# Optimization experiments

Hardware: AMD Instinct MI355X
Metric: run time of the kernel (lower is better)

## Reference

```python
import jax, jax.numpy as jnp
import numpy as np

D_MODEL, D_K, D_V = 1024, 64, 64

def setup_inputs() -> dict:
    key = jax.random.key(0)
    ks = jax.random.split(key, 7)
    s = 1.0 / np.sqrt(D_MODEL)
    return {
        "x": jax.random.normal(ks[0], (4, 4096, D_MODEL), dtype=jnp.float32),
        "w_q": jax.random.normal(ks[1], (D_MODEL, D_K), dtype=jnp.float32) * s,
        "b_q": jnp.zeros((D_K,), dtype=jnp.float32),
        "w_k": jax.random.normal(ks[2], (D_MODEL, D_K), dtype=jnp.float32) * s,
        "b_k": jnp.zeros((D_K,), dtype=jnp.float32),
        "w_v": jax.random.normal(ks[3], (D_MODEL, D_V), dtype=jnp.float32) * s,
        "b_v": jnp.zeros((D_V,), dtype=jnp.float32),
    }

def reference(x, w_q, b_q, w_k, b_k, w_v, b_v):
    # x: [b, s, d_model]
    q = x @ w_q + b_q                      # [b, s, d_k]
    k = x @ w_k + b_k                      # [b, s, d_k]
    v = x @ w_v + b_v                      # [b, s, d_v]
    scores = jnp.einsum("bqd,bkd->bqk", q, k) / jnp.sqrt(jnp.float32(D_K))
    seq_len = scores.shape[-1]
    causal = jnp.tril(jnp.ones((seq_len, seq_len), dtype=bool))  # keep lower-tri
    scores = jnp.where(causal, scores, -jnp.inf)
    probs = jax.nn.softmax(scores, axis=-1)
    return jnp.einsum("bqk,bkd->bqd", probs, v)  # [b, s, d_v]
```

## Files before the change

kernel.cpp:

```cpp
#include <hip/hip_runtime.h>
#include <hip/hip_bf16.h>

using f32x4    = __attribute__((ext_vector_type(4))) float;
using f32x16   = __attribute__((ext_vector_type(16))) float;
using bf16x8   = __attribute__((ext_vector_type(8))) __bf16;
using ushort8  = __attribute__((ext_vector_type(8))) unsigned short;
using ushort4v = __attribute__((ext_vector_type(4))) unsigned short;
using uint4v   = __attribute__((ext_vector_type(4))) unsigned int;
using float4v  = __attribute__((ext_vector_type(4))) float;

#define LOG2E 1.44269504088896340736f
#define SHIFT_L2 5.77078016355585f

static __device__ __forceinline__ unsigned short f2bf(float f) {
  union { __hip_bfloat16 h; unsigned short u; } cv;
  cv.h = __float2bfloat16(f);
  return cv.u;
}
static __device__ __forceinline__ bf16x8 ld_bf8_g(const void* p) {
  ushort8 u = *(const ushort8*)p;
  return __builtin_bit_cast(bf16x8, u);
}
static __device__ __forceinline__ float fast_exp2(float x) {
#if __has_builtin(__builtin_amdgcn_exp2f)
  return __builtin_amdgcn_exp2f(x);
#else
  return exp2f(x);
#endif
}
static __device__ __forceinline__ unsigned int pk2(float a, float b) {
  return (unsigned int)f2bf(a) | ((unsigned int)f2bf(b) << 16);
}

__global__ __launch_bounds__(256) void wprep_kernel(
    const float* __restrict__ wq, const float* __restrict__ wk,
    const float* __restrict__ wv, unsigned short* __restrict__ Wfrag) {
  int idx = blockIdx.x * 256 + threadIdx.x;
  int col = idx >> 10;
  int k   = idx & 1023;
  const float* w = (col < 64) ? wq : (col < 128) ? wk : wv;
  int c = col & 63;
  int n = col >> 4, l15 = col & 15;
  int kk = k >> 5, lh = (k >> 3) & 3, e = k & 7;
  size_t elem = ((size_t)(n * 32 + kk) * 64 + lh * 16 + l15) * 8 + e;
  Wfrag[elem] = f2bf(w[k * 64 + c]);
}

__global__ __launch_bounds__(256, 2) void proj_kernel(
    const float* __restrict__ x, const unsigned short* __restrict__ Wfrag,
    const float* __restrict__ bq, const float* __restrict__ bk,
    const float* __restrict__ bv,
    unsigned short* __restrict__ qb, unsigned short* __restrict__ kreg,
    unsigned short* __restrict__ vreg) {
  __shared__ __align__(16) char As[2][32 * 128];
  int tid = threadIdx.x, wave = tid >> 6, lane = tid & 63;
  int rowBase = blockIdx.x * 32;
  int rhalf = (wave & 1) * 16;
  int nbase = (wave >> 1) * 6;
  int l15 = lane & 15, lh = lane >> 4;

  int arow = tid >> 3, ac0 = (tid & 7) * 8;
  const float* xp = x + (size_t)(rowBase + arow) * 1024 + ac0;
  int abyte = (arow * 128 + ac0 * 2) ^ ((arow & 7) << 4);
  const char* wfb = (const char*)Wfrag + (size_t)lane * 16;

  f32x4 acc[6];
#pragma unroll
  for (int i = 0; i < 6; ++i) acc[i] = (f32x4){0.f, 0.f, 0.f, 0.f};

  float4v aL[2], aH[2];
  bf16x8 B[2][12];

  aL[0] = *(const float4v*)(xp);
  aH[0] = *(const float4v*)(xp + 4);
#pragma unroll
  for (int j = 0; j < 6; ++j) {
    B[0][j * 2]     = ld_bf8_g(wfb + (((size_t)(nbase + j) * 32 + 0) << 10));
    B[0][j * 2 + 1] = ld_bf8_g(wfb + (((size_t)(nbase + j) * 32 + 1) << 10));
  }
  {
    ushort8 u;
#pragma unroll
    for (int e = 0; e < 4; ++e) { u[e] = f2bf(aL[0][e]); u[4 + e] = f2bf(aH[0][e]); }
    *(ushort8*)(As[0] + abyte) = u;
  }
  aL[1] = *(const float4v*)(xp + 64);
  aH[1] = *(const float4v*)(xp + 68);
  asm volatile("s_waitcnt lgkmcnt(0)" ::: "memory");
  __builtin_amdgcn_s_barrier();
  __builtin_amdgcn_sched_barrier(0);

#pragma unroll
  for (int kt = 0; kt < 16; ++kt) {
    const int cur = kt & 1, nxt = cur ^ 1;
    if (kt < 15) {
#pragma unroll
      for (int j = 0; j < 6; ++j) {
        B[nxt][j * 2]     = ld_bf8_g(wfb + (((size_t)(nbase + j) * 32 + 2 * (kt + 1)) << 10));
        B[nxt][j * 2 + 1] = ld_bf8_g(wfb + (((size_t)(nbase + j) * 32 + 2 * (kt + 1) + 1) << 10));
      }
    }
    {
      int row = rhalf + l15;
      bf16x8 a0 = ld_bf8_g(As[cur] + ((row * 128 + lh * 16) ^ ((row & 7) << 4)));
      bf16x8 a1 = ld_bf8_g(As[cur] + ((row * 128 + 64 + lh * 16) ^ ((row & 7) << 4)));
#pragma unroll
      for (int j = 0; j < 6; ++j) {
        acc[j] = __builtin_amdgcn_mfma_f32_16x16x32_bf16(a0, B[cur][j * 2], acc[j], 0, 0, 0);
        acc[j] = __builtin_amdgcn_mfma_f32_16x16x32_bf16(a1, B[cur][j * 2 + 1], acc[j], 0, 0, 0);
      }
    }
    if (kt < 15) {
      ushort8 u;
#pragma unroll
      for (int e = 0; e < 4; ++e) { u[e] = f2bf(aL[nxt][e]); u[4 + e] = f2bf(aH[nxt][e]); }
      *(ushort8*)(As[nxt] + abyte) = u;
      if (kt < 14) {
        aL[cur] = *(const float4v*)(xp + (kt + 2) * 64);
        aH[cur] = *(const float4v*)(xp + (kt + 2) * 64 + 4);
      }
      asm volatile("s_waitcnt lgkmcnt(0)" ::: "memory");
      __builtin_amdgcn_s_barrier();
      __builtin_amdgcn_sched_barrier(0);
    }
  }

#pragma unroll
  for (int cf = 0; cf < 6; ++cf) {
    int col = (nbase + cf) * 16 + l15;
    int sel = col >> 6, c64 = col & 63;
    const float* bias = (sel == 0) ? bq : (sel == 1) ? bk : bv;
    float bb = bias[c64];
    if (sel == 0) {
#pragma unroll
      for (int r = 0; r < 4; ++r) {
        int row = rowBase + rhalf + lh * 4 + r;
        qb[(size_t)row * 64 + c64] = f2bf((acc[cf][r] + bb) * (0.125f * LOG2E));
      }
    } else if (sel == 1) {
      int j16 = c64 >> 4, hik = (c64 >> 3) & 1, e = c64 & 7;
#pragma unroll
      for (int r = 0; r < 4; ++r) {
        int s = rowBase + rhalf + lh * 4 + r;
        int b = s >> 12, sl = s & 4095;
        int ch = sl >> 7, kvw = sl & 127;
        int kvq = kvw >> 5, lk = kvw & 31;
        size_t off = (((size_t)(b * 32 + ch)) << 14) + kvq * 4096 + j16 * 1024 +
                     (hik * 32 + lk) * 16 + e * 2;
        *(unsigned short*)((char*)kreg + off) = f2bf(acc[cf][r] + bb);
      }
    } else {
      ushort4v w;
#pragma unroll
      for (int r = 0; r < 4; ++r) w[r] = f2bf(acc[cf][r] + bb);
      int s0 = rowBase + rhalf + lh * 4;
      int b = s0 >> 12, sl = s0 & 4095;
      int ch = sl >> 7, kvw = sl & 127;
      int kvq = kvw >> 5, k5 = kvw & 31;
      int kj = k5 >> 4, hiv = (k5 >> 3) & 1, e0 = k5 & 7;
      int dt = c64 >> 5, lv = c64 & 31, f = kj * 2 + dt;
      size_t off = (((size_t)(b * 32 + ch)) << 14) + kvq * 4096 + f * 1024 +
                   (hiv * 32 + lv) * 16 + e0 * 2;
      *(ushort4v*)((char*)vreg + off) = w;
    }
  }
}

__global__ __launch_bounds__(64, 4) void attn_kernel(
    const unsigned short* __restrict__ qb, const unsigned short* __restrict__ kreg,
    const unsigned short* __restrict__ vreg, float* __restrict__ po,
    float* __restrict__ lo) {
  int lane = threadIdx.x & 63;
  int l31 = lane & 31, hi = lane >> 5;
  int wid = blockIdx.x;
  int T = 127 - (wid >> 5);
  int low = wid & 31;
  int batch = low & 3, ph = low >> 2;
  int Tq = T * 32;
  const size_t bO = (size_t)batch * 262144;
  const char* kb = (const char*)kreg + ((size_t)batch << 19);
  const char* vb = (const char*)vreg + ((size_t)batch << 19);

  const unsigned short* qp = qb + bO + (size_t)(Tq + l31) * 64 + hi * 8;
  bf16x8 qf0 = ld_bf8_g(qp);
  bf16x8 qf1 = ld_bf8_g(qp + 16);
  bf16x8 qf2 = ld_bf8_g(qp + 32);
  bf16x8 qf3 = ld_bf8_g(qp + 48);

  f32x16 o0, o1;
#pragma unroll
  for (int r = 0; r < 16; ++r) { o0[r] = 0.f; o1[r] = 0.f; }
  float lsum = 0.f;

#pragma unroll 1
  for (int st = ph; st <= T; st += 8) {
    size_t base = ((size_t)(st >> 2) << 14) + (st & 3) * 4096 + lane * 16;
    const char* kp = kb + base;
    const char* vp = vb + base;
    bf16x8 k0 = ld_bf8_g(kp);
    bf16x8 k1 = ld_bf8_g(kp + 1024);
    bf16x8 k2 = ld_bf8_g(kp + 2048);
    bf16x8 k3 = ld_bf8_g(kp + 3072);
    bf16x8 v0 = ld_bf8_g(vp);
    bf16x8 v1 = ld_bf8_g(vp + 1024);
    bf16x8 v2 = ld_bf8_g(vp + 2048);
    bf16x8 v3 = ld_bf8_g(vp + 3072);

    f32x16 sc;
#pragma unroll
    for (int r = 0; r < 16; ++r) sc[r] = 0.f;
    sc = __builtin_amdgcn_mfma_f32_32x32x16_bf16(k0, qf0, sc, 0, 0, 0);
    sc = __builtin_amdgcn_mfma_f32_32x32x16_bf16(k1, qf1, sc, 0, 0, 0);
    sc = __builtin_amdgcn_mfma_f32_32x32x16_bf16(k2, qf2, sc, 0, 0, 0);
    sc = __builtin_amdgcn_mfma_f32_32x32x16_bf16(k3, qf3, sc, 0, 0, 0);
    if (st == T) {
      int qg = Tq + l31;
#pragma unroll
      for (int r = 0; r < 16; ++r) {
        int kvg = 32 * st + (r & 3) + 8 * (r >> 2) + 4 * hi;
        if (kvg > qg) sc[r] = -3.0e38f;
      }
    }
    float pv[16];
#pragma unroll
    for (int r = 0; r < 16; ++r) {
      pv[r] = fast_exp2(sc[r] - SHIFT_L2);
      lsum += pv[r];
    }
#pragma unroll
    for (int kj = 0; kj < 2; ++kj) {
      const int R = 8 * kj;
      unsigned int A0 = pk2(pv[R + 0], pv[R + 1]);
      unsigned int A1 = pk2(pv[R + 2], pv[R + 3]);
      unsigned int B0 = pk2(pv[R + 4], pv[R + 5]);
      unsigned int B1 = pk2(pv[R + 6], pv[R + 7]);
      unsigned int s0 = hi ? A0 : B0;
      unsigned int s1 = hi ? A1 : B1;
      unsigned int r0 = __shfl_xor((int)s0, 32, 64);
      unsigned int r1 = __shfl_xor((int)s1, 32, 64);
      uint4v dw = {hi ? r0 : A0, hi ? r1 : A1, hi ? B0 : r0, hi ? B1 : r1};
      bf16x8 pa = __builtin_bit_cast(bf16x8, dw);
      if (kj == 0) {
        o0 = __builtin_amdgcn_mfma_f32_32x32x16_bf16(pa, v0, o0, 0, 0, 0);
        o1 = __builtin_amdgcn_mfma_f32_32x32x16_bf16(pa, v1, o1, 0, 0, 0);
      } else {
        o0 = __builtin_amdgcn_mfma_f32_32x32x16_bf16(pa, v2, o0, 0, 0, 0);
        o1 = __builtin_amdgcn_mfma_f32_32x32x16_bf16(pa, v3, o1, 0, 0, 0);
      }
    }
  }

  lsum += __shfl_xor(lsum, 32, 64);

  float* pdst = po + (size_t)ph * 1048576 + bO + (size_t)Tq * 64;
#pragma unroll
  for (int r = 0; r < 16; ++r) {
    int qloc = (r & 3) + 8 * (r >> 2) + 4 * hi;
    pdst[qloc * 64 + l31] = o0[r];
    pdst[qloc * 64 + 32 + l31] = o1[r];
  }
  if (hi == 0) lo[ph * 16384 + batch * 4096 + Tq + l31] = lsum;
}

__global__ __launch_bounds__(256) void merge_kernel(
    const float* __restrict__ po, const float* __restrict__ lo,
    float* __restrict__ out) {
  int i = blockIdx.x * 256 + threadIdx.x;
  int row = i >> 4;
  float4v a = ((const float4v*)po)[i];
  float L = lo[row];
#pragma unroll
  for (int ph = 1; ph < 8; ++ph) {
    a += ((const float4v*)po)[i + ph * 262144];
    L += lo[row + ph * 16384];
  }
  a *= (1.0f / L);
  ((float4v*)out)[i] = a;
}

extern "C" void kernel_launch(void* const* d_in, const int* in_sizes, int n_in,
                              void* d_out, int out_size, void* d_ws, size_t ws_size,
                              hipStream_t stream) {
  const float* x  = (const float*)d_in[0];
  const float* wq = (const float*)d_in[1];
  const float* bq = (const float*)d_in[2];
  const float* wk = (const float*)d_in[3];
  const float* bk = (const float*)d_in[4];
  const float* wv = (const float*)d_in[5];
  const float* bv = (const float*)d_in[6];

  unsigned short* Wfrag = (unsigned short*)d_ws;
  unsigned short* qbuf  = Wfrag + 192 * 1024;
  unsigned short* kreg  = qbuf + 16384 * 64;
  unsigned short* vreg  = kreg + 16384 * 64;
  float*          po    = (float*)(vreg + 16384 * 64);
  float*          lo    = po + 8 * 1048576;

  wprep_kernel<<<768, 256, 0, stream>>>(wq, wk, wv, Wfrag);
  proj_kernel<<<512, 256, 0, stream>>>(x, Wfrag, bq, bk, bv, qbuf, kreg, vreg);
  attn_kernel<<<4096, 64, 0, stream>>>(qbuf, kreg, vreg, po, lo);
  merge_kernel<<<1024, 256, 0, stream>>>(po, lo, (float*)d_out);
}
```

Before: 55.45 us.

## Restructure projection GEMM into single-wave blocks with register-direct A loads

The projection kernel goes from 256-thread blocks that stage 32 rows of x in double-buffered LDS behind barriers to single-wave blocks of 16 rows. Each wave now computes all 192 output columns. Each lane loads its own fp32 x fragments from global memory with 4-deep register prefetch and converts them to bf16 in registers, and B fragments use 2-deep prefetch. This removes LDS traffic and block barriers, but doubles the weight-fragment reads from L2 per output row and leaves fewer waves per CU to hide memory latency.

```diff
diff --git a/kernel.cpp b/kernel.cpp
--- a/kernel.cpp
+++ b/kernel.cpp
@@ -46,102 +46,73 @@
   Wfrag[elem] = f2bf(w[k * 64 + c]);
 }
 
-__global__ __launch_bounds__(256, 2) void proj_kernel(
+__global__ __launch_bounds__(64, 2) void proj_kernel(
     const float* __restrict__ x, const unsigned short* __restrict__ Wfrag,
     const float* __restrict__ bq, const float* __restrict__ bk,
     const float* __restrict__ bv,
     unsigned short* __restrict__ qb, unsigned short* __restrict__ kreg,
     unsigned short* __restrict__ vreg) {
-  __shared__ __align__(16) char As[2][32 * 128];
-  int tid = threadIdx.x, wave = tid >> 6, lane = tid & 63;
-  int rowBase = blockIdx.x * 32;
-  int rhalf = (wave & 1) * 16;
-  int nbase = (wave >> 1) * 6;
+  int lane = threadIdx.x & 63;
   int l15 = lane & 15, lh = lane >> 4;
-
-  int arow = tid >> 3, ac0 = (tid & 7) * 8;
-  const float* xp = x + (size_t)(rowBase + arow) * 1024 + ac0;
-  int abyte = (arow * 128 + ac0 * 2) ^ ((arow & 7) << 4);
+  int rowBase = blockIdx.x * 16;
+  const float* xp = x + (size_t)(rowBase + l15) * 1024 + lh * 8;
   const char* wfb = (const char*)Wfrag + (size_t)lane * 16;
 
-  f32x4 acc[6];
-#pragma unroll
-  for (int i = 0; i < 6; ++i) acc[i] = (f32x4){0.f, 0.f, 0.f, 0.f};
-
-  float4v aL[2], aH[2];
-  bf16x8 B[2][12];
-
-  aL[0] = *(const float4v*)(xp);
-  aH[0] = *(const float4v*)(xp + 4);
-#pragma unroll
-  for (int j = 0; j < 6; ++j) {
-    B[0][j * 2]     = ld_bf8_g(wfb + (((size_t)(nbase + j) * 32 + 0) << 10));
-    B[0][j * 2 + 1] = ld_bf8_g(wfb + (((size_t)(nbase + j) * 32 + 1) << 10));
-  }
-  {
-    ushort8 u;
-#pragma unroll
-    for (int e = 0; e < 4; ++e) { u[e] = f2bf(aL[0][e]); u[4 + e] = f2bf(aH[0][e]); }
-    *(ushort8*)(As[0] + abyte) = u;
-  }
-  aL[1] = *(const float4v*)(xp + 64);
-  aH[1] = *(const float4v*)(xp + 68);
-  asm volatile("s_waitcnt lgkmcnt(0)" ::: "memory");
-  __builtin_amdgcn_s_barrier();
-  __builtin_amdgcn_sched_barrier(0);
-
-#pragma unroll
-  for (int kt = 0; kt < 16; ++kt) {
-    const int cur = kt & 1, nxt = cur ^ 1;
-    if (kt < 15) {
-#pragma unroll
-      for (int j = 0; j < 6; ++j) {
-        B[nxt][j * 2]     = ld_bf8_g(wfb + (((size_t)(nbase + j) * 32 + 2 * (kt + 1)) << 10));
-        B[nxt][j * 2 + 1] = ld_bf8_g(wfb + (((size_t)(nbase + j) * 32 + 2 * (kt + 1) + 1) << 10));
-      }
-    }
-    {
-      int row = rhalf + l15;
-      bf16x8 a0 = ld_bf8_g(As[cur] + ((row * 128 + lh * 16) ^ ((row & 7) << 4)));
-      bf16x8 a1 = ld_bf8_g(As[cur] + ((row * 128 + 64 + lh * 16) ^ ((row & 7) << 4)));
-#pragma unroll
-      for (int j = 0; j < 6; ++j) {
-        acc[j] = __builtin_amdgcn_mfma_f32_16x16x32_bf16(a0, B[cur][j * 2], acc[j], 0, 0, 0);
-        acc[j] = __builtin_amdgcn_mfma_f32_16x16x32_bf16(a1, B[cur][j * 2 + 1], acc[j], 0, 0, 0);
-      }
-    }
-    if (kt < 15) {
-      ushort8 u;
-#pragma unroll
-      for (int e = 0; e < 4; ++e) { u[e] = f2bf(aL[nxt][e]); u[4 + e] = f2bf(aH[nxt][e]); }
-      *(ushort8*)(As[nxt] + abyte) = u;
-      if (kt < 14) {
-        aL[cur] = *(const float4v*)(xp + (kt + 2) * 64);
-        aH[cur] = *(const float4v*)(xp + (kt + 2) * 64 + 4);
-      }
-      asm volatile("s_waitcnt lgkmcnt(0)" ::: "memory");
-      __builtin_amdgcn_s_barrier();
-      __builtin_amdgcn_sched_barrier(0);
-    }
-  }
-
-#pragma unroll
-  for (int cf = 0; cf < 6; ++cf) {
-    int col = (nbase + cf) * 16 + l15;
+  f32x4 acc[12];
+#pragma unroll
+  for (int i = 0; i < 12; ++i) acc[i] = (f32x4){0.f, 0.f, 0.f, 0.f};
+
+  float4v aL[4], aH[4];
+  bf16x8 Bb[2][12];
+
+#pragma unroll
+  for (int d = 0; d < 4; ++d) {
+    aL[d] = *(const float4v*)(xp + d * 32);
+    aH[d] = *(const float4v*)(xp + d * 32 + 4);
+  }
+#pragma unroll
+  for (int d = 0; d < 2; ++d)
+#pragma unroll
+    for (int j = 0; j < 12; ++j)
+      Bb[d][j] = ld_bf8_g(wfb + (((size_t)(j * 32 + d)) << 10));
+
+#pragma unroll
+  for (int kk = 0; kk < 32; ++kk) {
+    const int ab = kk & 3, bb = kk & 1;
+    uint4v au = {pk2(aL[ab][0], aL[ab][1]), pk2(aL[ab][2], aL[ab][3]),
+                 pk2(aH[ab][0], aH[ab][1]), pk2(aH[ab][2], aH[ab][3])};
+    bf16x8 af = __builtin_bit_cast(bf16x8, au);
+#pragma unroll
+    for (int j = 0; j < 12; ++j)
+      acc[j] = __builtin_amdgcn_mfma_f32_16x16x32_bf16(af, Bb[bb][j], acc[j], 0, 0, 0);
+    if (kk + 4 < 32) {
+      aL[ab] = *(const float4v*)(xp + (kk + 4) * 32);
+      aH[ab] = *(const float4v*)(xp + (kk + 4) * 32 + 4);
+    }
+    if (kk + 2 < 32) {
+#pragma unroll
+      for (int j = 0; j < 12; ++j)
+        Bb[bb][j] = ld_bf8_g(wfb + (((size_t)(j * 32 + kk + 2)) << 10));
+    }
+  }
+
+#pragma unroll
+  for (int cf = 0; cf < 12; ++cf) {
+    int col = cf * 16 + l15;
     int sel = col >> 6, c64 = col & 63;
     const float* bias = (sel == 0) ? bq : (sel == 1) ? bk : bv;
     float bb = bias[c64];
     if (sel == 0) {
 #pragma unroll
       for (int r = 0; r < 4; ++r) {
-        int row = rowBase + rhalf + lh * 4 + r;
+        int row = rowBase + lh * 4 + r;
         qb[(size_t)row * 64 + c64] = f2bf((acc[cf][r] + bb) * (0.125f * LOG2E));
       }
     } else if (sel == 1) {
       int j16 = c64 >> 4, hik = (c64 >> 3) & 1, e = c64 & 7;
 #pragma unroll
       for (int r = 0; r < 4; ++r) {
-        int s = rowBase + rhalf + lh * 4 + r;
+        int s = rowBase + lh * 4 + r;
         int b = s >> 12, sl = s & 4095;
         int ch = sl >> 7, kvw = sl & 127;
         int kvq = kvw >> 5, lk = kvw & 31;
@@ -153,7 +124,7 @@
       ushort4v w;
 #pragma unroll
       for (int r = 0; r < 4; ++r) w[r] = f2bf(acc[cf][r] + bb);
-      int s0 = rowBase + rhalf + lh * 4;
+      int s0 = rowBase + lh * 4;
       int b = s0 >> 12, sl = s0 & 4095;
       int ch = sl >> 7, kvw = sl & 127;
       int kvq = kvw >> 5, k5 = kvw & 31;
@@ -297,7 +268,7 @@
   float*          lo    = po + 8 * 1048576;
 
   wprep_kernel<<<768, 256, 0, stream>>>(wq, wk, wv, Wfrag);
-  proj_kernel<<<512, 256, 0, stream>>>(x, Wfrag, bq, bk, bv, qbuf, kreg, vreg);
+  proj_kernel<<<1024, 64, 0, stream>>>(x, Wfrag, bq, bk, bv, qbuf, kreg, vreg);
   attn_kernel<<<4096, 64, 0, stream>>>(qbuf, kreg, vreg, po, lo);
   merge_kernel<<<1024, 256, 0, stream>>>(po, lo, (float*)d_out);
 }
```

Result: slower. 61.80 us (+11.4%).
